# Performance work log

Measured on AMD Instinct MI355X. Metric: run time of the kernel, lower is better.

The kernel has to match this reference:

```python
import jax, jax.numpy as jnp
import numpy as np

HEADS = 16  # per module init; all heads share the same weights -> identical outputs


def setup_inputs() -> dict:
    key = jax.random.key(0)
    k1, k2, k3, k4 = jax.random.split(key, 4)
    B, S, E, HD = 8, 2048, 1024, 64  # embed_size=1024, heads=16, head_dim=64
    x = jax.random.normal(k1, (B, S, E), dtype=jnp.float32)
    Wq = jax.random.normal(k2, (HD, E), dtype=jnp.float32) * (E ** -0.5)
    Wk = jax.random.normal(k3, (HD, E), dtype=jnp.float32) * (E ** -0.5)
    Wv = jax.random.normal(k4, (HD, E), dtype=jnp.float32) * (E ** -0.5)
    return {"x": x, "Wq": Wq, "Wk": Wk, "Wv": Wv}


def reference(x, Wq, Wk, Wv):
    # Linear(embed, head_dim, bias=False): y = x @ W.T
    q = jnp.einsum('bse,de->bsd', x, Wq)  # [B,S,64]
    k = jnp.einsum('bse,de->bsd', x, Wk)
    v = jnp.einsum('bse,de->bsd', x, Wv)
    # scores [b, i(query), k(key)] -- NO scaling (scaled_factor unused in source)
    scores = jnp.einsum('bij,bkj->bik', q, k)
    # nn.Softmax(dim=1): normalize over the QUERY axis (axis=1), faithful quirk
    attn = jax.nn.softmax(scores, axis=1)
    out = jnp.matmul(attn, v)  # [B,S,64]
    # Per-head loop reuses identical weights -> concat == tile across heads
    return jnp.tile(out, (1, 1, HEADS))  # [B,S,1024]
```

## Files before the change

### kernel.cpp

```cpp
#include <hip/hip_runtime.h>

#define BATCH 8
#define SEQ   2048
#define EMB   1024
#define HD    64
#define HEADS 16
#define LOG2E 1.4426950408889634f

typedef _Float16 half8 __attribute__((ext_vector_type(8)));
typedef _Float16 half4 __attribute__((ext_vector_type(4)));
typedef float    f32x4 __attribute__((ext_vector_type(4)));

__device__ __forceinline__ float fexp2(float x) {
#if __has_builtin(__builtin_amdgcn_exp2f)
    return __builtin_amdgcn_exp2f(x);
#else
    return exp2f(x);
#endif
}

__device__ __forceinline__ void dma16(void* lds_base, const void* gsrc) {
    __builtin_amdgcn_global_load_lds(
        (const __attribute__((address_space(1))) unsigned int*)gsrc,
        (__attribute__((address_space(3))) unsigned int*)lds_base, 16, 0, 0);
}
__device__ __forceinline__ void dma4(void* lds_base, const void* gsrc) {
    __builtin_amdgcn_global_load_lds(
        (const __attribute__((address_space(1))) unsigned int*)gsrc,
        (__attribute__((address_space(3))) unsigned int*)lds_base, 4, 0, 0);
}

__global__ __launch_bounds__(256) void wcvt_kernel(
    const float* __restrict__ Wq, const float* __restrict__ Wk,
    const float* __restrict__ Wv, _Float16* __restrict__ Wh)
{
    const int m = blockIdx.y;
    const float* src = (m == 0) ? Wq : (m == 1) ? Wk : Wv;
    const float scale = (m == 0) ? LOG2E : 1.0f;
    const int idx = (blockIdx.x * 256 + threadIdx.x) * 8;
    float4 f0 = *(const float4*)(src + idx);
    float4 f1 = *(const float4*)(src + idx + 4);
    half8 h;
    h[0] = (_Float16)(f0.x * scale); h[1] = (_Float16)(f0.y * scale);
    h[2] = (_Float16)(f0.z * scale); h[3] = (_Float16)(f0.w * scale);
    h[4] = (_Float16)(f1.x * scale); h[5] = (_Float16)(f1.y * scale);
    h[6] = (_Float16)(f1.z * scale); h[7] = (_Float16)(f1.w * scale);
    *(half8*)(Wh + (size_t)m * 65536 + idx) = h;
}

__global__ __launch_bounds__(512) void qkv_kernel(
    const float* __restrict__ x, const _Float16* __restrict__ Wh,
    _Float16* __restrict__ qh, _Float16* __restrict__ kh, _Float16* __restrict__ vpt)
{
    __shared__ __align__(16) char arena[65536];
    const int t = threadIdx.x, lane = t & 63, wave = t >> 6;
    const int l15 = lane & 15, quad = lane >> 4;
    const int strip = wave & 1, grp = wave >> 1;
    const int row0 = blockIdx.x * 32;

    auto issue = [&](int buf, int k0) {
        #pragma unroll
        for (int jj = 0; jj < 4; ++jj) {
            const int j = wave * 4 + jj;
            if (j < 8) {
                const int row = j * 4 + (lane >> 4);
                const int logi = (lane & 15) ^ (row & 15);
                dma16((float*)(arena + buf * 8192) + j * 256,
                      x + (size_t)(row0 + row) * EMB + k0 + logi * 4);
            } else {
                const int jw = j - 8;
                const int dd = jw * 8 + (lane >> 3);
                const int logi = (lane & 7) ^ (dd & 7);
                dma16((_Float16*)(arena + 16384 + buf * 24576) + jw * 512,
                      Wh + (size_t)(dd >> 6) * 65536 + (size_t)(dd & 63) * EMB
                         + k0 + logi * 8);
            }
        }
    };

    issue(0, 0);
    __syncthreads();

    f32x4 acc[3] = {};
    const int xrow = strip * 16 + l15;
    for (int it = 0; it < 16; ++it) {
        const int buf = it & 1;
        if (it + 1 < 16) issue(buf ^ 1, (it + 1) * 64);
        const float* xb = (const float*)(arena + buf * 8192);
        const _Float16* wb = (const _Float16*)(arena + 16384 + buf * 24576);
        half8 a[2];
        #pragma unroll
        for (int kc = 0; kc < 2; ++kc) {
            const int s0 = kc * 8 + quad * 2;
            f32x4 u0 = *(const f32x4*)(xb + xrow * 64 + ((s0    ) ^ (l15 & 15)) * 4);
            f32x4 u1 = *(const f32x4*)(xb + xrow * 64 + ((s0 + 1) ^ (l15 & 15)) * 4);
            a[kc][0] = (_Float16)u0[0]; a[kc][1] = (_Float16)u0[1];
            a[kc][2] = (_Float16)u0[2]; a[kc][3] = (_Float16)u0[3];
            a[kc][4] = (_Float16)u1[0]; a[kc][5] = (_Float16)u1[1];
            a[kc][6] = (_Float16)u1[2]; a[kc][7] = (_Float16)u1[3];
        }
        #pragma unroll
        for (int j = 0; j < 3; ++j) {
            const int dd = (grp * 3 + j) * 16 + l15;
            #pragma unroll
            for (int kc = 0; kc < 2; ++kc) {
                half8 bfr = *(const half8*)(wb + dd * 64
                              + (((kc * 4 + quad) ^ (l15 & 7)) * 8));
                acc[j] = __builtin_amdgcn_mfma_f32_16x16x32_f16(a[kc], bfr, acc[j], 0, 0, 0);
            }
        }
        __syncthreads();
    }

    #pragma unroll
    for (int j = 0; j < 3; ++j) {
        const int c = grp * 3 + j, m = c >> 2, n = c & 3;
        if (m < 2) {
            _Float16* __restrict__ dst = (m == 0) ? qh : kh;
            #pragma unroll
            for (int r = 0; r < 4; ++r)
                dst[(size_t)(row0 + strip * 16 + quad * 4 + r) * HD + n * 16 + l15] =
                    (_Float16)acc[j][r];
        } else {
            const int rg = row0 + strip * 16 + quad * 4;
            const int b = rg >> 11, s = rg & 2047;
            half4 h;
            h[0] = (_Float16)acc[j][0]; h[1] = (_Float16)acc[j][1];
            h[2] = (_Float16)acc[j][2]; h[3] = (_Float16)acc[j][3];
            *(half4*)(vpt + ((size_t)b * HD + n * 16 + l15) * SEQ + s) = h;
        }
    }
}

__global__ __launch_bounds__(256) void stats_kernel(
    const _Float16* __restrict__ qh, const _Float16* __restrict__ kh,
    float* __restrict__ l_inv)
{
    __shared__ __align__(16) char arena[16384];
    __shared__ float red[4][32];
    const int t = threadIdx.x, lane = t & 63, wave = t >> 6;
    const int l15 = lane & 15, quad = lane >> 4;
    const int b = blockIdx.y, c0 = blockIdx.x * 32;

    half8 ka[2][2];
    #pragma unroll
    for (int kt = 0; kt < 2; ++kt) {
        const _Float16* kp = kh + ((size_t)b * SEQ + c0 + kt * 16 + l15) * HD + quad * 8;
        ka[kt][0] = *(const half8*)(kp);
        ka[kt][1] = *(const half8*)(kp + 32);
    }

    auto issue = [&](int buf, int q0) {
        #pragma unroll
        for (int jj = 0; jj < 2; ++jj) {
            const int j = wave * 2 + jj;
            const int qq = j * 8 + (lane >> 3);
            const int logi = (lane & 7) ^ (qq & 7);
            dma16((_Float16*)(arena + buf * 8192) + j * 512,
                  qh + ((size_t)b * SEQ + q0 + qq) * HD + logi * 8);
        }
    };

    issue(0, 0);
    __syncthreads();

    float csum[2][4] = {};
    const int qrow = wave * 16 + l15;
    for (int it = 0; it < 32; ++it) {
        const int buf = it & 1;
        if (it + 1 < 32) issue(buf ^ 1, (it + 1) * 64);
        const _Float16* qb = (const _Float16*)(arena + buf * 8192);
        half8 bq[2];
        #pragma unroll
        for (int kc = 0; kc < 2; ++kc)
            bq[kc] = *(const half8*)(qb + qrow * 64
                        + (((kc * 4 + quad) ^ (l15 & 7)) * 8));
        f32x4 s0 = {}, s1 = {};
        s0 = __builtin_amdgcn_mfma_f32_16x16x32_f16(ka[0][0], bq[0], s0, 0, 0, 0);
        s0 = __builtin_amdgcn_mfma_f32_16x16x32_f16(ka[0][1], bq[1], s0, 0, 0, 0);
        s1 = __builtin_amdgcn_mfma_f32_16x16x32_f16(ka[1][0], bq[0], s1, 0, 0, 0);
        s1 = __builtin_amdgcn_mfma_f32_16x16x32_f16(ka[1][1], bq[1], s1, 0, 0, 0);
        #pragma unroll
        for (int r = 0; r < 4; ++r) {
            csum[0][r] += fexp2(s0[r]);
            csum[1][r] += fexp2(s1[r]);
        }
        __syncthreads();
    }
    #pragma unroll
    for (int kt = 0; kt < 2; ++kt)
        #pragma unroll
        for (int r = 0; r < 4; ++r) {
            csum[kt][r] += __shfl_xor(csum[kt][r], 1);
            csum[kt][r] += __shfl_xor(csum[kt][r], 2);
            csum[kt][r] += __shfl_xor(csum[kt][r], 4);
            csum[kt][r] += __shfl_xor(csum[kt][r], 8);
        }
    if (l15 == 0) {
        #pragma unroll
        for (int kt = 0; kt < 2; ++kt)
            #pragma unroll
            for (int r = 0; r < 4; ++r)
                red[wave][kt * 16 + quad * 4 + r] = csum[kt][r];
    }
    __syncthreads();
    if (t < 32)
        l_inv[(size_t)b * SEQ + c0 + t] =
            1.0f / (red[0][t] + red[1][t] + red[2][t] + red[3][t]);
}

__global__ __launch_bounds__(256) void out_kernel(
    const _Float16* __restrict__ qh, const _Float16* __restrict__ kh,
    const _Float16* __restrict__ vpt, const float* __restrict__ l_inv,
    float* __restrict__ out)
{
    __shared__ __align__(16) char arena[38400];
    const int t = threadIdx.x, lane = t & 63, wave = t >> 6;
    const int l15 = lane & 15, quad = lane >> 4;
    const int rw = wave & 1, kw = wave >> 1;
    const int b = blockIdx.y, r0 = blockIdx.x * 32;

    half8 aq[2];
    {
        const _Float16* qp = qh + ((size_t)b * SEQ + r0 + rw * 16 + l15) * HD + quad * 8;
        aq[0] = *(const half8*)(qp);
        aq[1] = *(const half8*)(qp + 32);
    }

    auto issue = [&](int buf, int c0) {
        #pragma unroll
        for (int jj = 0; jj < 4; ++jj) {
            if (wave < 2) {
                const int j = wave * 4 + jj;
                const int key = j * 8 + (lane >> 3);
                const int logi = (lane & 7) ^ (key & 7);
                dma16((_Float16*)(arena + buf * 8192) + j * 512,
                      kh + ((size_t)b * SEQ + c0 + key) * HD + logi * 8);
            } else {
                const int j = (wave - 2) * 4 + jj;
                const int d = j * 8 + (lane >> 3);
                const int logi = (lane & 7) ^ (d & 7);
                dma16((_Float16*)(arena + 16384 + buf * 8192) + j * 512,
                      vpt + ((size_t)b * HD + d) * SEQ + c0 + logi * 8);
            }
        }
        if (wave == 0)
            dma4((float*)(arena + 32768) + buf * 64,
                 l_inv + (size_t)b * SEQ + c0 + lane);
    };

    issue(0, 0);
    __syncthreads();

    _Float16* psb = (_Float16*)(arena + 33280) + wave * 640;
    f32x4 oacc[4] = {};
    for (int it = 0; it < 32; ++it) {
        const int buf = it & 1;
        if (it + 1 < 32) issue(buf ^ 1, (it + 1) * 64);
        const _Float16* kb = (const _Float16*)(arena + buf * 8192);
        const _Float16* vb = (const _Float16*)(arena + 16384 + buf * 8192);
        const float*    lb = (const float*)(arena + 32768) + buf * 64;

        f32x4 s[2] = {};
        float li[2];
        #pragma unroll
        for (int ct = 0; ct < 2; ++ct) {
            const int key = kw * 32 + ct * 16 + l15;
            li[ct] = lb[key];
            #pragma unroll
            for (int kc = 0; kc < 2; ++kc) {
                half8 kf = *(const half8*)(kb + key * 64
                             + (((kc * 4 + quad) ^ (l15 & 7)) * 8));
                s[ct] = __builtin_amdgcn_mfma_f32_16x16x32_f16(aq[kc], kf, s[ct], 0, 0, 0);
            }
        }
        #pragma unroll
        for (int ct = 0; ct < 2; ++ct)
            #pragma unroll
            for (int r = 0; r < 4; ++r)
                psb[(quad * 4 + r) * 40 + ct * 16 + l15] =
                    (_Float16)(fexp2(s[ct][r]) * li[ct]);
        half8 pa = *(const half8*)(psb + l15 * 40 + quad * 8);
        #pragma unroll
        for (int n = 0; n < 4; ++n) {
            const int d = n * 16 + l15;
            half8 vf = *(const half8*)(vb + d * 64
                         + (((kw * 4 + quad) ^ (l15 & 7)) * 8));
            oacc[n] = __builtin_amdgcn_mfma_f32_16x16x32_f16(pa, vf, oacc[n], 0, 0, 0);
        }
        __syncthreads();
    }

    float* red = (float*)(arena);
    float* fin = (float*)(arena + 8704);
    if (kw == 1) {
        #pragma unroll
        for (int n = 0; n < 4; ++n)
            #pragma unroll
            for (int r = 0; r < 4; ++r)
                red[(rw * 16 + quad * 4 + r) * 68 + n * 16 + l15] = oacc[n][r];
    }
    __syncthreads();
    if (kw == 0) {
        #pragma unroll
        for (int n = 0; n < 4; ++n)
            #pragma unroll
            for (int r = 0; r < 4; ++r)
                fin[(rw * 16 + quad * 4 + r) * 68 + n * 16 + l15] =
                    oacc[n][r] + red[(rw * 16 + quad * 4 + r) * 68 + n * 16 + l15];
    }
    __syncthreads();

    const int row = t >> 3, s8 = t & 7;
    float4 u0 = *(float4*)(fin + row * 68 + s8 * 8);
    float4 u1 = *(float4*)(fin + row * 68 + s8 * 8 + 4);
    size_t base = ((size_t)b * SEQ + r0 + row) * (HD * HEADS);
    #pragma unroll
    for (int h = 0; h < HEADS; ++h) {
        *(float4*)&out[base + h * HD + s8 * 8]     = u0;
        *(float4*)&out[base + h * HD + s8 * 8 + 4] = u1;
    }
}

extern "C" void kernel_launch(void* const* d_in, const int* in_sizes, int n_in,
                              void* d_out, int out_size, void* d_ws, size_t ws_size,
                              hipStream_t stream)
{
    const float* x  = (const float*)d_in[0];
    const float* Wq = (const float*)d_in[1];
    const float* Wk = (const float*)d_in[2];
    const float* Wv = (const float*)d_in[3];
    float* out = (float*)d_out;

    const size_t N = (size_t)BATCH * SEQ * HD;
    _Float16* qh  = (_Float16*)d_ws;
    _Float16* kh  = qh + N;
    _Float16* vpt = kh + N;
    _Float16* Wh  = vpt + N;
    float* l_inv  = (float*)(Wh + 196608);

    wcvt_kernel <<<dim3(32, 3), 256, 0, stream>>>(Wq, Wk, Wv, Wh);
    qkv_kernel  <<<dim3(512),   512, 0, stream>>>(x, Wh, qh, kh, vpt);
    stats_kernel<<<dim3(64, 8), 256, 0, stream>>>(qh, kh, l_inv);
    out_kernel  <<<dim3(64, 8), 256, 0, stream>>>(qh, kh, vpt, l_inv, out);
}
```

Baseline: 178.4 us.

## Triple-buffer loads with vmcnt waits and fold softmax normalization into bf16 V

The qkv, stats and out kernels move from double-buffered loads with full __syncthreads to triple-buffered global_load_lds prefetch gated by explicit s_waitcnt vmcnt plus barrier. The stats kernel gives each wave its own private Q stream, so its main loop needs no barrier. It also pre-scales the transposed V by the inverse column sums in bf16, which removes the per-key l_inv load and multiply from the output kernel. V and P are now stored in bf16 and multiplied with bf16 MFMA, and occupancy hints are added via launch_bounds. This risks lower precision in V and P and more LDS use per block.

```diff
diff --git a/kernel.cpp b/kernel.cpp
--- a/kernel.cpp
+++ b/kernel.cpp
@@ -7,28 +7,31 @@
 #define HEADS 16
 #define LOG2E 1.4426950408889634f
 
-typedef _Float16 half8 __attribute__((ext_vector_type(8)));
-typedef _Float16 half4 __attribute__((ext_vector_type(4)));
-typedef float    f32x4 __attribute__((ext_vector_type(4)));
-
-__device__ __forceinline__ float fexp2(float x) {
-#if __has_builtin(__builtin_amdgcn_exp2f)
-    return __builtin_amdgcn_exp2f(x);
-#else
-    return exp2f(x);
-#endif
-}
-
-__device__ __forceinline__ void dma16(void* lds_base, const void* gsrc) {
+typedef _Float16 half8  __attribute__((ext_vector_type(8)));
+typedef short    short8v __attribute__((ext_vector_type(8)));
+typedef short    short4v __attribute__((ext_vector_type(4)));
+typedef float    f32x4  __attribute__((ext_vector_type(4)));
+
+__device__ __forceinline__ float fexp2(float x) { return __builtin_amdgcn_exp2f(x); }
+
+__device__ __forceinline__ short f2bf(float f) {
+    union { float f; unsigned u; } x; x.f = f;
+    unsigned r = x.u + 0x7fffu + ((x.u >> 16) & 1u);
+    return (short)(r >> 16);
+}
+__device__ __forceinline__ float bf2f(short s) {
+    union { unsigned u; float f; } x; x.u = ((unsigned)(unsigned short)s) << 16;
+    return x.f;
+}
+
+__device__ __forceinline__ void dma16(void* lds, const void* g) {
     __builtin_amdgcn_global_load_lds(
-        (const __attribute__((address_space(1))) unsigned int*)gsrc,
-        (__attribute__((address_space(3))) unsigned int*)lds_base, 16, 0, 0);
-}
-__device__ __forceinline__ void dma4(void* lds_base, const void* gsrc) {
-    __builtin_amdgcn_global_load_lds(
-        (const __attribute__((address_space(1))) unsigned int*)gsrc,
-        (__attribute__((address_space(3))) unsigned int*)lds_base, 4, 0, 0);
-}
+        (const __attribute__((address_space(1))) unsigned int*)g,
+        (__attribute__((address_space(3))) unsigned int*)lds, 16, 0, 0);
+}
+
+#define WAIT_BARRIER(N) asm volatile("s_waitcnt vmcnt(" #N ")\ns_barrier" ::: "memory")
+#define WAITVM(N)       asm volatile("s_waitcnt vmcnt(" #N ")" ::: "memory")
 
 __global__ __launch_bounds__(256) void wcvt_kernel(
     const float* __restrict__ Wq, const float* __restrict__ Wk,
@@ -48,30 +51,31 @@
     *(half8*)(Wh + (size_t)m * 65536 + idx) = h;
 }
 
-__global__ __launch_bounds__(512) void qkv_kernel(
+__global__ __launch_bounds__(512, 4) void qkv_kernel(
     const float* __restrict__ x, const _Float16* __restrict__ Wh,
-    _Float16* __restrict__ qh, _Float16* __restrict__ kh, _Float16* __restrict__ vpt)
-{
-    __shared__ __align__(16) char arena[65536];
+    _Float16* __restrict__ qh, _Float16* __restrict__ kh, short* __restrict__ vpt)
+{
+    __shared__ __align__(16) char arena[49152];
     const int t = threadIdx.x, lane = t & 63, wave = t >> 6;
     const int l15 = lane & 15, quad = lane >> 4;
     const int strip = wave & 1, grp = wave >> 1;
     const int row0 = blockIdx.x * 32;
 
     auto issue = [&](int buf, int k0) {
-        #pragma unroll
-        for (int jj = 0; jj < 4; ++jj) {
-            const int j = wave * 4 + jj;
-            if (j < 8) {
-                const int row = j * 4 + (lane >> 4);
-                const int logi = (lane & 15) ^ (row & 15);
-                dma16((float*)(arena + buf * 8192) + j * 256,
+        char* base = arena + buf * 16384;
+        #pragma unroll
+        for (int jj = 0; jj < 2; ++jj) {
+            const int j = wave * 2 + jj;
+            if (j < 4) {
+                const int row = j * 8 + (lane >> 3);
+                const int logi = (lane & 7) ^ (lane >> 3);
+                dma16(base + j * 1024,
                       x + (size_t)(row0 + row) * EMB + k0 + logi * 4);
             } else {
-                const int jw = j - 8;
-                const int dd = jw * 8 + (lane >> 3);
-                const int logi = (lane & 7) ^ (dd & 7);
-                dma16((_Float16*)(arena + 16384 + buf * 24576) + jw * 512,
+                const int jw = j - 4;
+                const int dd = jw * 16 + (lane >> 2);
+                const int logi = ((lane & 3) - ((lane >> 3) & 3)) & 3;
+                dma16(base + 4096 + jw * 1024,
                       Wh + (size_t)(dd >> 6) * 65536 + (size_t)(dd & 63) * EMB
                          + k0 + logi * 8);
             }
@@ -79,37 +83,29 @@
     };
 
     issue(0, 0);
-    __syncthreads();
+    issue(1, 32);
 
     f32x4 acc[3] = {};
     const int xrow = strip * 16 + l15;
-    for (int it = 0; it < 16; ++it) {
-        const int buf = it & 1;
-        if (it + 1 < 16) issue(buf ^ 1, (it + 1) * 64);
-        const float* xb = (const float*)(arena + buf * 8192);
-        const _Float16* wb = (const _Float16*)(arena + 16384 + buf * 24576);
-        half8 a[2];
-        #pragma unroll
-        for (int kc = 0; kc < 2; ++kc) {
-            const int s0 = kc * 8 + quad * 2;
-            f32x4 u0 = *(const f32x4*)(xb + xrow * 64 + ((s0    ) ^ (l15 & 15)) * 4);
-            f32x4 u1 = *(const f32x4*)(xb + xrow * 64 + ((s0 + 1) ^ (l15 & 15)) * 4);
-            a[kc][0] = (_Float16)u0[0]; a[kc][1] = (_Float16)u0[1];
-            a[kc][2] = (_Float16)u0[2]; a[kc][3] = (_Float16)u0[3];
-            a[kc][4] = (_Float16)u1[0]; a[kc][5] = (_Float16)u1[1];
-            a[kc][6] = (_Float16)u1[2]; a[kc][7] = (_Float16)u1[3];
-        }
+    for (int it = 0; it < 32; ++it) {
+        if (it < 31) { WAIT_BARRIER(2); } else { WAIT_BARRIER(0); }
+        if (it + 2 < 32) issue((it + 2) % 3, (it + 2) * 32);
+        const int buf = it % 3;
+        const float* xb = (const float*)(arena + buf * 16384);
+        const _Float16* wb = (const _Float16*)(arena + buf * 16384 + 4096);
+        f32x4 u0 = *(const f32x4*)(xb + xrow * 32 + (((quad * 2)     ^ (l15 & 7)) * 4));
+        f32x4 u1 = *(const f32x4*)(xb + xrow * 32 + (((quad * 2 + 1) ^ (l15 & 7)) * 4));
+        half8 a;
+        a[0] = (_Float16)u0[0]; a[1] = (_Float16)u0[1];
+        a[2] = (_Float16)u0[2]; a[3] = (_Float16)u0[3];
+        a[4] = (_Float16)u1[0]; a[5] = (_Float16)u1[1];
+        a[6] = (_Float16)u1[2]; a[7] = (_Float16)u1[3];
         #pragma unroll
         for (int j = 0; j < 3; ++j) {
             const int dd = (grp * 3 + j) * 16 + l15;
-            #pragma unroll
-            for (int kc = 0; kc < 2; ++kc) {
-                half8 bfr = *(const half8*)(wb + dd * 64
-                              + (((kc * 4 + quad) ^ (l15 & 7)) * 8));
-                acc[j] = __builtin_amdgcn_mfma_f32_16x16x32_f16(a[kc], bfr, acc[j], 0, 0, 0);
-            }
-        }
-        __syncthreads();
+            half8 bfr = *(const half8*)(wb + dd * 32 + (((quad + (dd >> 1)) & 3) * 8));
+            acc[j] = __builtin_amdgcn_mfma_f32_16x16x32_f16(a, bfr, acc[j], 0, 0, 0);
+        }
     }
 
     #pragma unroll
@@ -124,20 +120,21 @@
         } else {
             const int rg = row0 + strip * 16 + quad * 4;
             const int b = rg >> 11, s = rg & 2047;
-            half4 h;
-            h[0] = (_Float16)acc[j][0]; h[1] = (_Float16)acc[j][1];
-            h[2] = (_Float16)acc[j][2]; h[3] = (_Float16)acc[j][3];
-            *(half4*)(vpt + ((size_t)b * HD + n * 16 + l15) * SEQ + s) = h;
-        }
-    }
-}
-
-__global__ __launch_bounds__(256) void stats_kernel(
+            short4v h;
+            h[0] = f2bf(acc[j][0]); h[1] = f2bf(acc[j][1]);
+            h[2] = f2bf(acc[j][2]); h[3] = f2bf(acc[j][3]);
+            *(short4v*)(vpt + ((size_t)b * HD + n * 16 + l15) * SEQ + s) = h;
+        }
+    }
+}
+
+__global__ __launch_bounds__(256, 2) void stats_kernel(
     const _Float16* __restrict__ qh, const _Float16* __restrict__ kh,
-    float* __restrict__ l_inv)
-{
-    __shared__ __align__(16) char arena[16384];
+    short* __restrict__ vpt)
+{
+    __shared__ __align__(16) char arena[49152];
     __shared__ float red[4][32];
+    __shared__ float linv_s[32];
     const int t = threadIdx.x, lane = t & 63, wave = t >> 6;
     const int l15 = lane & 15, quad = lane >> 4;
     const int b = blockIdx.y, c0 = blockIdx.x * 32;
@@ -150,42 +147,44 @@
         ka[kt][1] = *(const half8*)(kp + 32);
     }
 
+    char* mybase = arena + wave * 12288;
     auto issue = [&](int buf, int q0) {
         #pragma unroll
-        for (int jj = 0; jj < 2; ++jj) {
-            const int j = wave * 2 + jj;
+        for (int j = 0; j < 4; ++j) {
             const int qq = j * 8 + (lane >> 3);
-            const int logi = (lane & 7) ^ (qq & 7);
-            dma16((_Float16*)(arena + buf * 8192) + j * 512,
+            const int logi = (lane & 7) ^ (lane >> 3);
+            dma16(mybase + buf * 4096 + j * 1024,
                   qh + ((size_t)b * SEQ + q0 + qq) * HD + logi * 8);
         }
     };
 
-    issue(0, 0);
-    __syncthreads();
+    const int q0w = wave * 512;
+    issue(0, q0w);
+    issue(1, q0w + 32);
 
     float csum[2][4] = {};
-    const int qrow = wave * 16 + l15;
-    for (int it = 0; it < 32; ++it) {
-        const int buf = it & 1;
-        if (it + 1 < 32) issue(buf ^ 1, (it + 1) * 64);
-        const _Float16* qb = (const _Float16*)(arena + buf * 8192);
-        half8 bq[2];
-        #pragma unroll
-        for (int kc = 0; kc < 2; ++kc)
-            bq[kc] = *(const half8*)(qb + qrow * 64
-                        + (((kc * 4 + quad) ^ (l15 & 7)) * 8));
-        f32x4 s0 = {}, s1 = {};
-        s0 = __builtin_amdgcn_mfma_f32_16x16x32_f16(ka[0][0], bq[0], s0, 0, 0, 0);
-        s0 = __builtin_amdgcn_mfma_f32_16x16x32_f16(ka[0][1], bq[1], s0, 0, 0, 0);
-        s1 = __builtin_amdgcn_mfma_f32_16x16x32_f16(ka[1][0], bq[0], s1, 0, 0, 0);
-        s1 = __builtin_amdgcn_mfma_f32_16x16x32_f16(ka[1][1], bq[1], s1, 0, 0, 0);
-        #pragma unroll
-        for (int r = 0; r < 4; ++r) {
-            csum[0][r] += fexp2(s0[r]);
-            csum[1][r] += fexp2(s1[r]);
-        }
-        __syncthreads();
+    for (int it = 0; it < 16; ++it) {
+        if (it < 15) { WAITVM(4); } else { WAITVM(0); }
+        if (it + 2 < 16) issue((it + 2) % 3, q0w + (it + 2) * 32);
+        const _Float16* qb = (const _Float16*)(mybase + (it % 3) * 4096);
+        #pragma unroll
+        for (int qt = 0; qt < 2; ++qt) {
+            half8 bq[2];
+            #pragma unroll
+            for (int kc = 0; kc < 2; ++kc)
+                bq[kc] = *(const half8*)(qb + (qt * 16 + l15) * 64
+                           + (((kc * 4 + quad) ^ (l15 & 7)) * 8));
+            f32x4 s0 = {}, s1 = {};
+            s0 = __builtin_amdgcn_mfma_f32_16x16x32_f16(ka[0][0], bq[0], s0, 0, 0, 0);
+            s0 = __builtin_amdgcn_mfma_f32_16x16x32_f16(ka[0][1], bq[1], s0, 0, 0, 0);
+            s1 = __builtin_amdgcn_mfma_f32_16x16x32_f16(ka[1][0], bq[0], s1, 0, 0, 0);
+            s1 = __builtin_amdgcn_mfma_f32_16x16x32_f16(ka[1][1], bq[1], s1, 0, 0, 0);
+            #pragma unroll
+            for (int r = 0; r < 4; ++r) {
+                csum[0][r] += fexp2(s0[r]);
+                csum[1][r] += fexp2(s1[r]);
+            }
+        }
     }
     #pragma unroll
     for (int kt = 0; kt < 2; ++kt)
@@ -205,16 +204,24 @@
     }
     __syncthreads();
     if (t < 32)
-        l_inv[(size_t)b * SEQ + c0 + t] =
-            1.0f / (red[0][t] + red[1][t] + red[2][t] + red[3][t]);
-}
-
-__global__ __launch_bounds__(256) void out_kernel(
+        linv_s[t] = 1.0f / (red[0][t] + red[1][t] + red[2][t] + red[3][t]);
+    __syncthreads();
+    {
+        const int d = t >> 2, sg = (t & 3) * 8;
+        short* vp = vpt + ((size_t)b * HD + d) * SEQ + c0 + sg;
+        short8v vv = *(short8v*)vp, ro;
+        #pragma unroll
+        for (int j = 0; j < 8; ++j)
+            ro[j] = f2bf(bf2f(vv[j]) * linv_s[sg + j]);
+        *(short8v*)vp = ro;
+    }
+}
+
+__global__ __launch_bounds__(256, 2) void out_kernel(
     const _Float16* __restrict__ qh, const _Float16* __restrict__ kh,
-    const _Float16* __restrict__ vpt, const float* __restrict__ l_inv,
-    float* __restrict__ out)
-{
-    __shared__ __align__(16) char arena[38400];
+    const short* __restrict__ vpt, float* __restrict__ out)
+{
+    __shared__ __align__(16) char arena[54272];
     const int t = threadIdx.x, lane = t & 63, wave = t >> 6;
     const int l15 = lane & 15, quad = lane >> 4;
     const int rw = wave & 1, kw = wave >> 1;
@@ -228,45 +235,40 @@
     }
 
     auto issue = [&](int buf, int c0) {
+        char* base = arena + buf * 16384;
         #pragma unroll
         for (int jj = 0; jj < 4; ++jj) {
-            if (wave < 2) {
-                const int j = wave * 4 + jj;
+            const int j = wave * 4 + jj;
+            const int logi = (lane & 7) ^ (lane >> 3);
+            if (j < 8) {
                 const int key = j * 8 + (lane >> 3);
-                const int logi = (lane & 7) ^ (key & 7);
-                dma16((_Float16*)(arena + buf * 8192) + j * 512,
+                dma16(base + j * 1024,
                       kh + ((size_t)b * SEQ + c0 + key) * HD + logi * 8);
             } else {
-                const int j = (wave - 2) * 4 + jj;
-                const int d = j * 8 + (lane >> 3);
-                const int logi = (lane & 7) ^ (d & 7);
-                dma16((_Float16*)(arena + 16384 + buf * 8192) + j * 512,
+                const int jv = j - 8;
+                const int d = jv * 8 + (lane >> 3);
+                dma16(base + 8192 + jv * 1024,
                       vpt + ((size_t)b * HD + d) * SEQ + c0 + logi * 8);
             }
         }
-        if (wave == 0)
-            dma4((float*)(arena + 32768) + buf * 64,
-                 l_inv + (size_t)b * SEQ + c0 + lane);
     };
 
     issue(0, 0);
-    __syncthreads();
-
-    _Float16* psb = (_Float16*)(arena + 33280) + wave * 640;
+    issue(1, 64);
+
+    short* psb = (short*)(arena + 49152) + wave * 640;
     f32x4 oacc[4] = {};
     for (int it = 0; it < 32; ++it) {
-        const int buf = it & 1;
-        if (it + 1 < 32) issue(buf ^ 1, (it + 1) * 64);
-        const _Float16* kb = (const _Float16*)(arena + buf * 8192);
-        const _Float16* vb = (const _Float16*)(arena + 16384 + buf * 8192);
-        const float*    lb = (const float*)(arena + 32768) + buf * 64;
+        if (it < 31) { WAIT_BARRIER(4); } else { WAIT_BARRIER(0); }
+        if (it + 2 < 32) issue((it + 2) % 3, (it + 2) * 64);
+        const int buf = it % 3;
+        const _Float16* kb = (const _Float16*)(arena + buf * 16384);
+        const short* vb = (const short*)(arena + buf * 16384 + 8192);
 
         f32x4 s[2] = {};
-        float li[2];
         #pragma unroll
         for (int ct = 0; ct < 2; ++ct) {
             const int key = kw * 32 + ct * 16 + l15;
-            li[ct] = lb[key];
             #pragma unroll
             for (int kc = 0; kc < 2; ++kc) {
                 half8 kf = *(const half8*)(kb + key * 64
@@ -278,20 +280,19 @@
         for (int ct = 0; ct < 2; ++ct)
             #pragma unroll
             for (int r = 0; r < 4; ++r)
-                psb[(quad * 4 + r) * 40 + ct * 16 + l15] =
-                    (_Float16)(fexp2(s[ct][r]) * li[ct]);
-        half8 pa = *(const half8*)(psb + l15 * 40 + quad * 8);
+                psb[(quad * 4 + r) * 40 + ct * 16 + l15] = f2bf(fexp2(s[ct][r]));
+        short8v pa = *(const short8v*)(psb + l15 * 40 + quad * 8);
         #pragma unroll
         for (int n = 0; n < 4; ++n) {
             const int d = n * 16 + l15;
-            half8 vf = *(const half8*)(vb + d * 64
-                         + (((kw * 4 + quad) ^ (l15 & 7)) * 8));
-            oacc[n] = __builtin_amdgcn_mfma_f32_16x16x32_f16(pa, vf, oacc[n], 0, 0, 0);
-        }
-        __syncthreads();
-    }
-
-    float* red = (float*)(arena);
+            short8v vf = *(const short8v*)(vb + d * 64
+                           + (((kw * 4 + quad) ^ (l15 & 7)) * 8));
+            oacc[n] = __builtin_amdgcn_mfma_f32_16x16x32_bf16(pa, vf, oacc[n], 0, 0, 0);
+        }
+    }
+    __syncthreads();
+
+    float* red = (float*)arena;
     float* fin = (float*)(arena + 8704);
     if (kw == 1) {
         #pragma unroll
@@ -335,12 +336,11 @@
     const size_t N = (size_t)BATCH * SEQ * HD;
     _Float16* qh  = (_Float16*)d_ws;
     _Float16* kh  = qh + N;
-    _Float16* vpt = kh + N;
-    _Float16* Wh  = vpt + N;
-    float* l_inv  = (float*)(Wh + 196608);
+    short*    vpt = (short*)(kh + N);
+    _Float16* Wh  = (_Float16*)(vpt + N);
 
     wcvt_kernel <<<dim3(32, 3), 256, 0, stream>>>(Wq, Wk, Wv, Wh);
     qkv_kernel  <<<dim3(512),   512, 0, stream>>>(x, Wh, qh, kh, vpt);
-    stats_kernel<<<dim3(64, 8), 256, 0, stream>>>(qh, kh, l_inv);
-    out_kernel  <<<dim3(64, 8), 256, 0, stream>>>(qh, kh, vpt, l_inv, out);
-}
+    stats_kernel<<<dim3(64, 8), 256, 0, stream>>>(qh, kh, vpt);
+    out_kernel  <<<dim3(64, 8), 256, 0, stream>>>(qh, kh, vpt, out);
+}
```

Measured after the change: 181.2 us. About the same (+1.6%).
